# Kernel optimization log

Measured on AMD Instinct MI355X. Metric: run time of the kernel, lower is better.

The kernel has to match this reference:

```python
import jax, jax.numpy as jnp
import numpy as np

H = 256  # GRU hidden size (self.dim)

def setup_inputs() -> dict:
    key = jax.random.key(0)
    ks = jax.random.split(key, 7)
    B, T, N_IN, N_C = 256, 512, 512, 101
    s_ih = 1.0 / np.sqrt(H)
    x    = jax.random.normal(ks[0], (B, T, N_IN), dtype=jnp.float32)
    W_ih = jax.random.uniform(ks[1], (3 * H, N_IN), minval=-s_ih, maxval=s_ih, dtype=jnp.float32)
    W_hh = jax.random.uniform(ks[2], (3 * H, H),    minval=-s_ih, maxval=s_ih, dtype=jnp.float32)
    b_ih = jax.random.uniform(ks[3], (3 * H,), minval=-s_ih, maxval=s_ih, dtype=jnp.float32)
    b_hh = jax.random.uniform(ks[4], (3 * H,), minval=-s_ih, maxval=s_ih, dtype=jnp.float32)
    s_fc = 1.0 / np.sqrt(H)
    fc_w = jax.random.uniform(ks[5], (N_C, H), minval=-s_fc, maxval=s_fc, dtype=jnp.float32)
    fc_b = jax.random.uniform(ks[6], (N_C,),   minval=-s_fc, maxval=s_fc, dtype=jnp.float32)
    return {"x": x, "W_ih": W_ih, "W_hh": W_hh, "b_ih": b_ih, "b_hh": b_hh,
            "fc_w": fc_w, "fc_b": fc_b}

def _gru_last_hidden(x, W_ih, W_hh, b_ih, b_hh):
    B = x.shape[0]
    # Precompute input-side gate projections for all timesteps: [B, T, 3H]
    xg = jnp.einsum('bti,gi->btg', x, W_ih) + b_ih
    h0 = jnp.zeros((B, H), dtype=x.dtype)

    def step(h, xg_t):
        hg = h @ W_hh.T + b_hh                      # [B, 3H]
        xr, xz, xn = jnp.split(xg_t, 3, axis=-1)    # PyTorch gate order: r, z, n
        hr, hz, hn = jnp.split(hg, 3, axis=-1)
        r = jax.nn.sigmoid(xr + hr)
        z = jax.nn.sigmoid(xz + hz)
        n = jnp.tanh(xn + r * hn)
        h_new = (1.0 - z) * n + z * h
        return h_new, None

    hT, _ = jax.lax.scan(step, h0, jnp.swapaxes(xg, 0, 1))  # scan over T
    return hT  # [B, H]

def reference(x, W_ih, W_hh, b_ih, b_hh, fc_w, fc_b):
    hT = _gru_last_hidden(x, W_ih, W_hh, b_ih, b_hh)
    return hT @ fc_w.T + fc_b  # [B, n_c]
```

## Files before the change

### kernel.cpp

```cpp
#include <hip/hip_runtime.h>
#include <hip/hip_bf16.h>
#include <cstdint>
#include <cstddef>

typedef __attribute__((ext_vector_type(4))) float floatx4;
typedef __attribute__((ext_vector_type(8))) short shortx8;
typedef __attribute__((ext_vector_type(2))) __fp16 f16x2;

#define T_SEQ 512
#define NIN   512
#define BATCH 256
#define HID   256
#define G3    768
#define NC    101

static __device__ __forceinline__ unsigned short f2bf(float f){
  unsigned int u = __float_as_uint(f);
  u += 0x7FFFu + ((u >> 16) & 1u);
  return (unsigned short)(u >> 16);
}

static __device__ __forceinline__ float dot2acc(f16x2 w, f16x2 h, float acc){
#if __has_builtin(__builtin_amdgcn_fdot2)
  return __builtin_amdgcn_fdot2(w, h, acc, false);
#else
  return acc + (float)w[0]*(float)h[0] + (float)w[1]*(float)h[1];
#endif
}

#define BM 128
#define BN 128
#define BK 64
#define LDK 72

__global__ __launch_bounds__(256) void gemm_xg(
    const float* __restrict__ x, const float* __restrict__ Wih,
    const float* __restrict__ bih, float* __restrict__ xg,
    int t0, int tcLog2)
{
  __shared__ unsigned short As[BM*LDK];
  __shared__ unsigned short Bs[BN*LDK];
  const int tid  = threadIdx.x;
  const int bn   = blockIdx.x;
  const int bm   = blockIdx.y;
  const int w    = tid >> 6;
  const int l    = tid & 63;
  const int lm   = l & 15;
  const int quad = l >> 4;

  const int srow = tid >> 4;
  const int scol = (tid & 15) * 4;
  const int tcMask = (1 << tcLog2) - 1;

  floatx4 acc[2][8];
  #pragma unroll
  for (int mt = 0; mt < 2; ++mt)
    #pragma unroll
    for (int nt = 0; nt < 8; ++nt)
      acc[mt][nt] = (floatx4){0.f, 0.f, 0.f, 0.f};

  for (int kt = 0; kt < NIN / BK; ++kt){
    const int k0 = kt * BK;
    __syncthreads();
    #pragma unroll
    for (int p = 0; p < 8; ++p){
      const int r  = p * 16 + srow;
      const int gm = bm * BM + r;
      const int b  = gm >> tcLog2;
      const int tt = gm & tcMask;
      const float4 xa = *(const float4*)(x + (size_t)(b * T_SEQ + t0 + tt) * NIN + k0 + scol);
      union { unsigned short u[4]; uint2 v; } pa;
      pa.u[0] = f2bf(xa.x); pa.u[1] = f2bf(xa.y); pa.u[2] = f2bf(xa.z); pa.u[3] = f2bf(xa.w);
      *(uint2*)&As[r * LDK + scol] = pa.v;
      const int gn = bn * BN + r;
      const float4 wb = *(const float4*)(Wih + (size_t)gn * NIN + k0 + scol);
      union { unsigned short u[4]; uint2 v; } pb;
      pb.u[0] = f2bf(wb.x); pb.u[1] = f2bf(wb.y); pb.u[2] = f2bf(wb.z); pb.u[3] = f2bf(wb.w);
      *(uint2*)&Bs[r * LDK + scol] = pb.v;
    }
    __syncthreads();
    #pragma unroll
    for (int ks = 0; ks < 2; ++ks){
      const int kk = ks * 32 + quad * 8;
      shortx8 af[2], bfr[8];
      #pragma unroll
      for (int mt = 0; mt < 2; ++mt)
        af[mt] = *(const shortx8*)&As[(w * 32 + mt * 16 + lm) * LDK + kk];
      #pragma unroll
      for (int nt = 0; nt < 8; ++nt)
        bfr[nt] = *(const shortx8*)&Bs[(nt * 16 + lm) * LDK + kk];
      #pragma unroll
      for (int mt = 0; mt < 2; ++mt)
        #pragma unroll
        for (int nt = 0; nt < 8; ++nt)
          acc[mt][nt] = __builtin_amdgcn_mfma_f32_16x16x32_bf16(af[mt], bfr[nt], acc[mt][nt], 0, 0, 0);
    }
  }

  #pragma unroll
  for (int mt = 0; mt < 2; ++mt){
    #pragma unroll
    for (int nt = 0; nt < 8; ++nt){
      #pragma unroll
      for (int i = 0; i < 4; ++i){
        const int ml = w * 32 + mt * 16 + quad * 4 + i;
        const int nl = nt * 16 + lm;
        const int gm = bm * BM + ml;
        const int gn = bn * BN + nl;
        xg[(size_t)gm * G3 + gn] = acc[mt][nt][i] + bih[gn];
      }
    }
  }
}

#define HSTRIDE 280

__global__ __launch_bounds__(512, 2) void gru_steps(
    const float* __restrict__ xg, const float* __restrict__ Whh,
    const float* __restrict__ bhh, float* __restrict__ hstate, int Tc)
{
  __shared__ alignas(16) unsigned short hph[2][HSTRIDE];
  const int b    = blockIdx.x;
  const int tid  = threadIdx.x;
  const int j    = tid >> 1;
  const int half = tid & 1;
  const int jpos = j + (j >= 128 ? 8 : 0);

  f16x2 wrr[64], wrz[64], wrn[64];
  {
    const float4* r4 = (const float4*)(Whh + (size_t)j * HID + half * 128);
    const float4* z4 = (const float4*)(Whh + (size_t)(j + 256) * HID + half * 128);
    const float4* n4 = (const float4*)(Whh + (size_t)(j + 512) * HID + half * 128);
    #pragma unroll
    for (int k = 0; k < 32; ++k){
      float4 v = r4[k];
      wrr[2*k]   = __builtin_amdgcn_cvt_pkrtz(v.x, v.y);
      wrr[2*k+1] = __builtin_amdgcn_cvt_pkrtz(v.z, v.w);
    }
    #pragma unroll
    for (int k = 0; k < 32; ++k){
      float4 v = z4[k];
      wrz[2*k]   = __builtin_amdgcn_cvt_pkrtz(v.x, v.y);
      wrz[2*k+1] = __builtin_amdgcn_cvt_pkrtz(v.z, v.w);
    }
    #pragma unroll
    for (int k = 0; k < 32; ++k){
      float4 v = n4[k];
      wrn[2*k]   = __builtin_amdgcn_cvt_pkrtz(v.x, v.y);
      wrn[2*k+1] = __builtin_amdgcn_cvt_pkrtz(v.z, v.w);
    }
  }
  const float br = bhh[j];
  const float bz = bhh[j + 256];
  const float bn = bhh[j + 512];

  float hj = hstate[b * HID + j];
  if (half == 0){
    union { __fp16 f; unsigned short u; } cv;
    cv.f = (__fp16)hj;
    hph[0][jpos] = cv.u;
  }
  __syncthreads();

  const float* xgrow = xg + (size_t)b * Tc * G3 + j;
  float xr = xgrow[0], xz = xgrow[256], xn = xgrow[512];

  #pragma unroll 1
  for (int t = 0; t < Tc; ++t){
    const int tn = (t + 1 < Tc) ? (t + 1) : t;
    const float nxr = xgrow[(size_t)tn * G3];
    const float nxz = xgrow[(size_t)tn * G3 + 256];
    const float nxn = xgrow[(size_t)tn * G3 + 512];

    const uint4* hp4 = (const uint4*)(&hph[t & 1][0]) + half * 17;
    uint4 hv[16];
    #pragma unroll
    for (int i = 0; i < 16; ++i) hv[i] = hp4[i];

    float ar = 0.f, az = 0.f, an = 0.f;
    #pragma unroll
    for (int i = 0; i < 16; ++i){
      union { unsigned int u; f16x2 h; } c0, c1, c2, c3;
      c0.u = hv[i].x; c1.u = hv[i].y; c2.u = hv[i].z; c3.u = hv[i].w;
      const int p = 4 * i;
      ar = dot2acc(wrr[p    ], c0.h, ar);
      az = dot2acc(wrz[p    ], c0.h, az);
      an = dot2acc(wrn[p    ], c0.h, an);
      ar = dot2acc(wrr[p + 1], c1.h, ar);
      az = dot2acc(wrz[p + 1], c1.h, az);
      an = dot2acc(wrn[p + 1], c1.h, an);
      ar = dot2acc(wrr[p + 2], c2.h, ar);
      az = dot2acc(wrz[p + 2], c2.h, az);
      an = dot2acc(wrn[p + 2], c2.h, an);
      ar = dot2acc(wrr[p + 3], c3.h, ar);
      az = dot2acc(wrz[p + 3], c3.h, az);
      an = dot2acc(wrn[p + 3], c3.h, an);
    }
    const float hr = ar + __shfl_xor(ar, 1, 64) + br;
    const float hz = az + __shfl_xor(az, 1, 64) + bz;
    const float hn = an + __shfl_xor(an, 1, 64) + bn;

    const float r = 1.f / (1.f + __expf(-(xr + hr)));
    const float z = 1.f / (1.f + __expf(-(xz + hz)));
    const float a = xn + r * hn;
    const float ex = __expf(-2.f * fabsf(a));
    float n = (1.f - ex) / (1.f + ex);
    n = copysignf(n, a);
    const float hnew = fmaf(z, hj - n, n);

    hj = hnew;
    if (half == 0){
      union { __fp16 f; unsigned short u; } cv;
      cv.f = (__fp16)hj;
      hph[1 - (t & 1)][jpos] = cv.u;
    }
    __syncthreads();
    xr = nxr; xz = nxz; xn = nxn;
  }

  if (half == 0) hstate[b * HID + j] = hj;
}

__global__ __launch_bounds__(128) void fc_kernel(
    const float* __restrict__ hstate, const float* __restrict__ fw,
    const float* __restrict__ fb, float* __restrict__ out)
{
  __shared__ float hs[HID];
  const int b = blockIdx.x;
  const int t = threadIdx.x;
  hs[t]       = hstate[b * HID + t];
  hs[t + 128] = hstate[b * HID + t + 128];
  __syncthreads();
  if (t < NC){
    float acc = fb[t];
    const float4* w4 = (const float4*)(fw + (size_t)t * HID);
    const float4* h4 = (const float4*)hs;
    #pragma unroll
    for (int k = 0; k < 64; ++k){
      const float4 wv = w4[k];
      const float4 hv = h4[k];
      acc += wv.x * hv.x + wv.y * hv.y + wv.z * hv.z + wv.w * hv.w;
    }
    out[b * NC + t] = acc;
  }
}

extern "C" void kernel_launch(void* const* d_in, const int* in_sizes, int n_in,
                              void* d_out, int out_size, void* d_ws, size_t ws_size,
                              hipStream_t stream)
{
  const float* x   = (const float*)d_in[0];
  const float* Wih = (const float*)d_in[1];
  const float* Whh = (const float*)d_in[2];
  const float* bih = (const float*)d_in[3];
  const float* bhh = (const float*)d_in[4];
  const float* fcw = (const float*)d_in[5];
  const float* fcb = (const float*)d_in[6];
  float* out = (float*)d_out;

  float* hst = (float*)d_ws;
  const size_t hBytes = (size_t)BATCH * HID * sizeof(float);
  float* xg  = (float*)((char*)d_ws + hBytes);

  const size_t perT = (size_t)BATCH * G3 * sizeof(float);
  const size_t avail = (ws_size > hBytes) ? (ws_size - hBytes) : 0;
  int tcLog2 = 9;
  while (tcLog2 > 0 && perT * ((size_t)1 << tcLog2) > avail) --tcLog2;
  const int Tc = 1 << tcLog2;

  (void)hipMemsetAsync(hst, 0, hBytes, stream);
  for (int t0 = 0; t0 < T_SEQ; t0 += Tc){
    dim3 grid(6, 2 * Tc);
    gemm_xg<<<grid, 256, 0, stream>>>(x, Wih, bih, xg, t0, tcLog2);
    gru_steps<<<BATCH, 512, 0, stream>>>(xg, Whh, bhh, hst, Tc);
  }
  fc_kernel<<<BATCH, 128, 0, stream>>>(hst, fcw, fcb, out);
}
```

Before: 1.281 ms.

## Split GRU recurrent dot products across four lanes with DPP reduction

Reworks the per-step recurrent matvec so each group of four lanes computes two hidden units. Each lane covers a 64-wide K slice and the partial sums are combined with two DPP adds instead of one ds_swizzle shuffle. Each lane now reads half as much of the f16 hidden state from LDS per step, and each h value is reused across six weight rows instead of three. The cost is more duplicated work: every lane computes six accumulators and redundant gate math for two outputs, and the LDS padding layout changes.

```diff
diff --git a/kernel.cpp b/kernel.cpp
--- a/kernel.cpp
+++ b/kernel.cpp
@@ -26,6 +26,12 @@
 #else
   return acc + (float)w[0]*(float)h[0] + (float)w[1]*(float)h[1];
 #endif
+}
+
+template<int CTRL>
+static __device__ __forceinline__ float dppadd(float v){
+  return v + __int_as_float(__builtin_amdgcn_update_dpp(
+      0, __float_as_int(v), CTRL, 0xF, 0xF, true));
 }
 
 #define BM 128
@@ -120,85 +126,110 @@
     const float* __restrict__ bhh, float* __restrict__ hstate, int Tc)
 {
   __shared__ alignas(16) unsigned short hph[2][HSTRIDE];
-  const int b    = blockIdx.x;
-  const int tid  = threadIdx.x;
-  const int j    = tid >> 1;
-  const int half = tid & 1;
-  const int jpos = j + (j >= 128 ? 8 : 0);
-
-  f16x2 wrr[64], wrz[64], wrn[64];
+  const int b   = blockIdx.x;
+  const int tid = threadIdx.x;
+  const int q   = tid & 3;
+  const int g   = tid >> 2;
+  const int sel = q >> 1;
+  const int jm  = g + (sel << 7);
+  const int k0  = q << 6;
+
+  f16x2 w0r[32], w0z[32], w0n[32], w1r[32], w1z[32], w1n[32];
   {
-    const float4* r4 = (const float4*)(Whh + (size_t)j * HID + half * 128);
-    const float4* z4 = (const float4*)(Whh + (size_t)(j + 256) * HID + half * 128);
-    const float4* n4 = (const float4*)(Whh + (size_t)(j + 512) * HID + half * 128);
-    #pragma unroll
-    for (int k = 0; k < 32; ++k){
-      float4 v = r4[k];
-      wrr[2*k]   = __builtin_amdgcn_cvt_pkrtz(v.x, v.y);
-      wrr[2*k+1] = __builtin_amdgcn_cvt_pkrtz(v.z, v.w);
-    }
-    #pragma unroll
-    for (int k = 0; k < 32; ++k){
-      float4 v = z4[k];
-      wrz[2*k]   = __builtin_amdgcn_cvt_pkrtz(v.x, v.y);
-      wrz[2*k+1] = __builtin_amdgcn_cvt_pkrtz(v.z, v.w);
-    }
-    #pragma unroll
-    for (int k = 0; k < 32; ++k){
-      float4 v = n4[k];
-      wrn[2*k]   = __builtin_amdgcn_cvt_pkrtz(v.x, v.y);
-      wrn[2*k+1] = __builtin_amdgcn_cvt_pkrtz(v.z, v.w);
-    }
-  }
-  const float br = bhh[j];
-  const float bz = bhh[j + 256];
-  const float bn = bhh[j + 512];
-
-  float hj = hstate[b * HID + j];
-  if (half == 0){
+    const float4* p0 = (const float4*)(Whh + (size_t)(g      ) * HID + k0);
+    #pragma unroll
+    for (int k = 0; k < 16; ++k){ float4 v = p0[k];
+      w0r[2*k] = __builtin_amdgcn_cvt_pkrtz(v.x, v.y); w0r[2*k+1] = __builtin_amdgcn_cvt_pkrtz(v.z, v.w); }
+    const float4* p1 = (const float4*)(Whh + (size_t)(g + 256) * HID + k0);
+    #pragma unroll
+    for (int k = 0; k < 16; ++k){ float4 v = p1[k];
+      w0z[2*k] = __builtin_amdgcn_cvt_pkrtz(v.x, v.y); w0z[2*k+1] = __builtin_amdgcn_cvt_pkrtz(v.z, v.w); }
+    const float4* p2 = (const float4*)(Whh + (size_t)(g + 512) * HID + k0);
+    #pragma unroll
+    for (int k = 0; k < 16; ++k){ float4 v = p2[k];
+      w0n[2*k] = __builtin_amdgcn_cvt_pkrtz(v.x, v.y); w0n[2*k+1] = __builtin_amdgcn_cvt_pkrtz(v.z, v.w); }
+    const float4* p3 = (const float4*)(Whh + (size_t)(g + 128) * HID + k0);
+    #pragma unroll
+    for (int k = 0; k < 16; ++k){ float4 v = p3[k];
+      w1r[2*k] = __builtin_amdgcn_cvt_pkrtz(v.x, v.y); w1r[2*k+1] = __builtin_amdgcn_cvt_pkrtz(v.z, v.w); }
+    const float4* p4 = (const float4*)(Whh + (size_t)(g + 384) * HID + k0);
+    #pragma unroll
+    for (int k = 0; k < 16; ++k){ float4 v = p4[k];
+      w1z[2*k] = __builtin_amdgcn_cvt_pkrtz(v.x, v.y); w1z[2*k+1] = __builtin_amdgcn_cvt_pkrtz(v.z, v.w); }
+    const float4* p5 = (const float4*)(Whh + (size_t)(g + 640) * HID + k0);
+    #pragma unroll
+    for (int k = 0; k < 16; ++k){ float4 v = p5[k];
+      w1n[2*k] = __builtin_amdgcn_cvt_pkrtz(v.x, v.y); w1n[2*k+1] = __builtin_amdgcn_cvt_pkrtz(v.z, v.w); }
+  }
+  const float br = bhh[jm];
+  const float bz = bhh[jm + 256];
+  const float bn = bhh[jm + 512];
+
+  float hj = hstate[b * HID + jm];
+  const int wpos = jm + ((jm >> 6) << 3);
+  if (!(q & 1)){
     union { __fp16 f; unsigned short u; } cv;
     cv.f = (__fp16)hj;
-    hph[0][jpos] = cv.u;
+    hph[0][wpos] = cv.u;
   }
   __syncthreads();
 
-  const float* xgrow = xg + (size_t)b * Tc * G3 + j;
-  float xr = xgrow[0], xz = xgrow[256], xn = xgrow[512];
+  const int xbase = b * Tc * G3 + jm;
+  float xr = xg[xbase], xz = xg[xbase + 256], xn = xg[xbase + 512];
 
   #pragma unroll 1
   for (int t = 0; t < Tc; ++t){
     const int tn = (t + 1 < Tc) ? (t + 1) : t;
-    const float nxr = xgrow[(size_t)tn * G3];
-    const float nxz = xgrow[(size_t)tn * G3 + 256];
-    const float nxn = xgrow[(size_t)tn * G3 + 512];
-
-    const uint4* hp4 = (const uint4*)(&hph[t & 1][0]) + half * 17;
-    uint4 hv[16];
-    #pragma unroll
-    for (int i = 0; i < 16; ++i) hv[i] = hp4[i];
-
-    float ar = 0.f, az = 0.f, an = 0.f;
-    #pragma unroll
-    for (int i = 0; i < 16; ++i){
+    const int xo = xbase + tn * G3;
+    const float nxr = xg[xo];
+    const float nxz = xg[xo + 256];
+    const float nxn = xg[xo + 512];
+
+    const uint4* hp4 = (const uint4*)(&hph[t & 1][0]) + 9 * q;
+    uint4 hv[8];
+    #pragma unroll
+    for (int i = 0; i < 8; ++i) hv[i] = hp4[i];
+
+    float a0r = 0.f, a0z = 0.f, a0n = 0.f, a1r = 0.f, a1z = 0.f, a1n = 0.f;
+    #pragma unroll
+    for (int i = 0; i < 8; ++i){
       union { unsigned int u; f16x2 h; } c0, c1, c2, c3;
       c0.u = hv[i].x; c1.u = hv[i].y; c2.u = hv[i].z; c3.u = hv[i].w;
       const int p = 4 * i;
-      ar = dot2acc(wrr[p    ], c0.h, ar);
-      az = dot2acc(wrz[p    ], c0.h, az);
-      an = dot2acc(wrn[p    ], c0.h, an);
-      ar = dot2acc(wrr[p + 1], c1.h, ar);
-      az = dot2acc(wrz[p + 1], c1.h, az);
-      an = dot2acc(wrn[p + 1], c1.h, an);
-      ar = dot2acc(wrr[p + 2], c2.h, ar);
-      az = dot2acc(wrz[p + 2], c2.h, az);
-      an = dot2acc(wrn[p + 2], c2.h, an);
-      ar = dot2acc(wrr[p + 3], c3.h, ar);
-      az = dot2acc(wrz[p + 3], c3.h, az);
-      an = dot2acc(wrn[p + 3], c3.h, an);
-    }
-    const float hr = ar + __shfl_xor(ar, 1, 64) + br;
-    const float hz = az + __shfl_xor(az, 1, 64) + bz;
-    const float hn = an + __shfl_xor(an, 1, 64) + bn;
+      a0r = dot2acc(w0r[p    ], c0.h, a0r);
+      a0z = dot2acc(w0z[p    ], c0.h, a0z);
+      a0n = dot2acc(w0n[p    ], c0.h, a0n);
+      a1r = dot2acc(w1r[p    ], c0.h, a1r);
+      a1z = dot2acc(w1z[p    ], c0.h, a1z);
+      a1n = dot2acc(w1n[p    ], c0.h, a1n);
+      a0r = dot2acc(w0r[p + 1], c1.h, a0r);
+      a0z = dot2acc(w0z[p + 1], c1.h, a0z);
+      a0n = dot2acc(w0n[p + 1], c1.h, a0n);
+      a1r = dot2acc(w1r[p + 1], c1.h, a1r);
+      a1z = dot2acc(w1z[p + 1], c1.h, a1z);
+      a1n = dot2acc(w1n[p + 1], c1.h, a1n);
+      a0r = dot2acc(w0r[p + 2], c2.h, a0r);
+      a0z = dot2acc(w0z[p + 2], c2.h, a0z);
+      a0n = dot2acc(w0n[p + 2], c2.h, a0n);
+      a1r = dot2acc(w1r[p + 2], c2.h, a1r);
+      a1z = dot2acc(w1z[p + 2], c2.h, a1z);
+      a1n = dot2acc(w1n[p + 2], c2.h, a1n);
+      a0r = dot2acc(w0r[p + 3], c3.h, a0r);
+      a0z = dot2acc(w0z[p + 3], c3.h, a0z);
+      a0n = dot2acc(w0n[p + 3], c3.h, a0n);
+      a1r = dot2acc(w1r[p + 3], c3.h, a1r);
+      a1z = dot2acc(w1z[p + 3], c3.h, a1z);
+      a1n = dot2acc(w1n[p + 3], c3.h, a1n);
+    }
+
+    a0r = dppadd<0xB1>(a0r); a0z = dppadd<0xB1>(a0z); a0n = dppadd<0xB1>(a0n);
+    a1r = dppadd<0xB1>(a1r); a1z = dppadd<0xB1>(a1z); a1n = dppadd<0xB1>(a1n);
+    a0r = dppadd<0x4E>(a0r); a0z = dppadd<0x4E>(a0z); a0n = dppadd<0x4E>(a0n);
+    a1r = dppadd<0x4E>(a1r); a1z = dppadd<0x4E>(a1z); a1n = dppadd<0x4E>(a1n);
+
+    const float hr = (sel ? a1r : a0r) + br;
+    const float hz = (sel ? a1z : a0z) + bz;
+    const float hn = (sel ? a1n : a0n) + bn;
 
     const float r = 1.f / (1.f + __expf(-(xr + hr)));
     const float z = 1.f / (1.f + __expf(-(xz + hz)));
@@ -209,16 +240,16 @@
     const float hnew = fmaf(z, hj - n, n);
 
     hj = hnew;
-    if (half == 0){
+    if (!(q & 1)){
       union { __fp16 f; unsigned short u; } cv;
       cv.f = (__fp16)hj;
-      hph[1 - (t & 1)][jpos] = cv.u;
+      hph[1 - (t & 1)][wpos] = cv.u;
     }
     __syncthreads();
     xr = nxr; xz = nxz; xn = nxn;
   }
 
-  if (half == 0) hstate[b * HID + j] = hj;
+  if (!(q & 1)) hstate[b * HID + jm] = hj;
 }
 
 __global__ __launch_bounds__(128) void fc_kernel(
```

Result: faster. 1.255 ms (-2.0%).

## Batch GRU recurrence over 16 sequences per block using MFMA, store xg in fp16

Applied to the files above, without the earlier changes.

Replaces the per-sequence dot2 recurrence (one block per batch row) with a block that handles 16 batch rows and computes the hidden-to-hidden product with 16x16x32 f16 MFMA. W_hh fragments stay in registers and h is kept swizzled in LDS. The input projection buffer is also written in fp16, halving its memory traffic. Only 16 blocks now run the recurrence, so parallelism drops sharply and per-step latency becomes the deciding cost. fp16 storage of xg also adds rounding error.

```diff
diff --git a/kernel.cpp b/kernel.cpp
--- a/kernel.cpp
+++ b/kernel.cpp
@@ -1,11 +1,13 @@
 #include <hip/hip_runtime.h>
 #include <hip/hip_bf16.h>
+#include <hip/hip_fp16.h>
 #include <cstdint>
 #include <cstddef>
 
 typedef __attribute__((ext_vector_type(4))) float floatx4;
 typedef __attribute__((ext_vector_type(8))) short shortx8;
 typedef __attribute__((ext_vector_type(2))) __fp16 f16x2;
+typedef __attribute__((ext_vector_type(8))) __fp16 halfx8;
 
 #define T_SEQ 512
 #define NIN   512
@@ -20,14 +22,6 @@
   return (unsigned short)(u >> 16);
 }
 
-static __device__ __forceinline__ float dot2acc(f16x2 w, f16x2 h, float acc){
-#if __has_builtin(__builtin_amdgcn_fdot2)
-  return __builtin_amdgcn_fdot2(w, h, acc, false);
-#else
-  return acc + (float)w[0]*(float)h[0] + (float)w[1]*(float)h[1];
-#endif
-}
-
 #define BM 128
 #define BN 128
 #define BK 64
@@ -35,7 +29,7 @@
 
 __global__ __launch_bounds__(256) void gemm_xg(
     const float* __restrict__ x, const float* __restrict__ Wih,
-    const float* __restrict__ bih, float* __restrict__ xg,
+    const float* __restrict__ bih, __fp16* __restrict__ xg,
     int t0, int tcLog2)
 {
   __shared__ unsigned short As[BM*LDK];
@@ -107,118 +101,135 @@
         const int nl = nt * 16 + lm;
         const int gm = bm * BM + ml;
         const int gn = bn * BN + nl;
-        xg[(size_t)gm * G3 + gn] = acc[mt][nt][i] + bih[gn];
+        xg[(size_t)gm * G3 + gn] = (__fp16)(acc[mt][nt][i] + bih[gn]);
       }
     }
   }
 }
 
-#define HSTRIDE 280
-
-__global__ __launch_bounds__(512, 2) void gru_steps(
-    const float* __restrict__ xg, const float* __restrict__ Whh,
+#define BB 16
+
+__global__ __launch_bounds__(512, 2) void gru_mfma(
+    const __fp16* __restrict__ xg, const float* __restrict__ Whh,
     const float* __restrict__ bhh, float* __restrict__ hstate, int Tc)
 {
-  __shared__ alignas(16) unsigned short hph[2][HSTRIDE];
-  const int b    = blockIdx.x;
-  const int tid  = threadIdx.x;
-  const int j    = tid >> 1;
-  const int half = tid & 1;
-  const int jpos = j + (j >= 128 ? 8 : 0);
-
-  f16x2 wrr[64], wrz[64], wrn[64];
-  {
-    const float4* r4 = (const float4*)(Whh + (size_t)j * HID + half * 128);
-    const float4* z4 = (const float4*)(Whh + (size_t)(j + 256) * HID + half * 128);
-    const float4* n4 = (const float4*)(Whh + (size_t)(j + 512) * HID + half * 128);
-    #pragma unroll
-    for (int k = 0; k < 32; ++k){
-      float4 v = r4[k];
-      wrr[2*k]   = __builtin_amdgcn_cvt_pkrtz(v.x, v.y);
-      wrr[2*k+1] = __builtin_amdgcn_cvt_pkrtz(v.z, v.w);
-    }
-    #pragma unroll
-    for (int k = 0; k < 32; ++k){
-      float4 v = z4[k];
-      wrz[2*k]   = __builtin_amdgcn_cvt_pkrtz(v.x, v.y);
-      wrz[2*k+1] = __builtin_amdgcn_cvt_pkrtz(v.z, v.w);
-    }
-    #pragma unroll
-    for (int k = 0; k < 32; ++k){
-      float4 v = n4[k];
-      wrn[2*k]   = __builtin_amdgcn_cvt_pkrtz(v.x, v.y);
-      wrn[2*k+1] = __builtin_amdgcn_cvt_pkrtz(v.z, v.w);
-    }
-  }
-  const float br = bhh[j];
-  const float bz = bhh[j + 256];
-  const float bn = bhh[j + 512];
-
-  float hj = hstate[b * HID + j];
-  if (half == 0){
-    union { __fp16 f; unsigned short u; } cv;
-    cv.f = (__fp16)hj;
-    hph[0][jpos] = cv.u;
-  }
+  __shared__ __align__(16) __fp16 hls[2][BB * HID];
+  const int tid = threadIdx.x;
+  const int w   = tid >> 6;
+  const int l   = tid & 63;
+  const int lm  = l & 15;
+  const int lq  = l >> 4;
+  const int bb0 = blockIdx.x * BB;
+  const int jb  = w * 32 + lm;
+  const int hswz = (lm & 7) << 3;
+
+  halfx8 Bf[3][2][8];
+  #pragma unroll
+  for (int g = 0; g < 3; ++g)
+    #pragma unroll
+    for (int js = 0; js < 2; ++js)
+      #pragma unroll
+      for (int ks = 0; ks < 8; ++ks){
+        const float* wp = Whh + (size_t)(g * 256 + w * 32 + js * 16 + lm) * HID + ks * 32 + lq * 8;
+        const float4 v0 = *(const float4*)wp;
+        const float4 v1 = *(const float4*)(wp + 4);
+        union { f16x2 h[4]; halfx8 v; } u;
+        u.h[0] = __builtin_amdgcn_cvt_pkrtz(v0.x, v0.y);
+        u.h[1] = __builtin_amdgcn_cvt_pkrtz(v0.z, v0.w);
+        u.h[2] = __builtin_amdgcn_cvt_pkrtz(v1.x, v1.y);
+        u.h[3] = __builtin_amdgcn_cvt_pkrtz(v1.z, v1.w);
+        Bf[g][js][ks] = u.v;
+      }
+
+  float bias[3][2];
+  #pragma unroll
+  for (int g = 0; g < 3; ++g){
+    bias[g][0] = bhh[g * 256 + jb];
+    bias[g][1] = bhh[g * 256 + jb + 16];
+  }
+
+  float hold[2][4];
+  #pragma unroll
+  for (int js = 0; js < 2; ++js)
+    #pragma unroll
+    for (int i = 0; i < 4; ++i){
+      const int b = lq * 4 + i;
+      const int j = jb + js * 16;
+      const float h0 = hstate[(bb0 + b) * HID + j];
+      hold[js][i] = h0;
+      hls[0][b * HID + (j ^ ((b & 7) << 3))] = (__fp16)h0;
+    }
+
+  int rowoff[4];
+  #pragma unroll
+  for (int i = 0; i < 4; ++i)
+    rowoff[i] = ((bb0 + lq * 4 + i) * Tc) * G3 + jb;
+
   __syncthreads();
-
-  const float* xgrow = xg + (size_t)b * Tc * G3 + j;
-  float xr = xgrow[0], xz = xgrow[256], xn = xgrow[512];
 
   #pragma unroll 1
   for (int t = 0; t < Tc; ++t){
-    const int tn = (t + 1 < Tc) ? (t + 1) : t;
-    const float nxr = xgrow[(size_t)tn * G3];
-    const float nxz = xgrow[(size_t)tn * G3 + 256];
-    const float nxn = xgrow[(size_t)tn * G3 + 512];
-
-    const uint4* hp4 = (const uint4*)(&hph[t & 1][0]) + half * 17;
-    uint4 hv[16];
-    #pragma unroll
-    for (int i = 0; i < 16; ++i) hv[i] = hp4[i];
-
-    float ar = 0.f, az = 0.f, an = 0.f;
-    #pragma unroll
-    for (int i = 0; i < 16; ++i){
-      union { unsigned int u; f16x2 h; } c0, c1, c2, c3;
-      c0.u = hv[i].x; c1.u = hv[i].y; c2.u = hv[i].z; c3.u = hv[i].w;
-      const int p = 4 * i;
-      ar = dot2acc(wrr[p    ], c0.h, ar);
-      az = dot2acc(wrz[p    ], c0.h, az);
-      an = dot2acc(wrn[p    ], c0.h, an);
-      ar = dot2acc(wrr[p + 1], c1.h, ar);
-      az = dot2acc(wrz[p + 1], c1.h, az);
-      an = dot2acc(wrn[p + 1], c1.h, an);
-      ar = dot2acc(wrr[p + 2], c2.h, ar);
-      az = dot2acc(wrz[p + 2], c2.h, az);
-      an = dot2acc(wrn[p + 2], c2.h, an);
-      ar = dot2acc(wrr[p + 3], c3.h, ar);
-      az = dot2acc(wrz[p + 3], c3.h, az);
-      an = dot2acc(wrn[p + 3], c3.h, an);
-    }
-    const float hr = ar + __shfl_xor(ar, 1, 64) + br;
-    const float hz = az + __shfl_xor(az, 1, 64) + bz;
-    const float hn = an + __shfl_xor(an, 1, 64) + bn;
-
-    const float r = 1.f / (1.f + __expf(-(xr + hr)));
-    const float z = 1.f / (1.f + __expf(-(xz + hz)));
-    const float a = xn + r * hn;
-    const float ex = __expf(-2.f * fabsf(a));
-    float n = (1.f - ex) / (1.f + ex);
-    n = copysignf(n, a);
-    const float hnew = fmaf(z, hj - n, n);
-
-    hj = hnew;
-    if (half == 0){
-      union { __fp16 f; unsigned short u; } cv;
-      cv.f = (__fp16)hj;
-      hph[1 - (t & 1)][jpos] = cv.u;
-    }
+    __fp16 xv[3][2][4];
+    #pragma unroll
+    for (int i = 0; i < 4; ++i){
+      const __fp16* xp = xg + rowoff[i] + t * G3;
+      #pragma unroll
+      for (int g = 0; g < 3; ++g)
+        #pragma unroll
+        for (int js = 0; js < 2; ++js)
+          xv[g][js][i] = xp[g * 256 + js * 16];
+    }
+
+    floatx4 acc[3][2];
+    #pragma unroll
+    for (int g = 0; g < 3; ++g)
+      #pragma unroll
+      for (int js = 0; js < 2; ++js)
+        acc[g][js] = (floatx4){bias[g][js], bias[g][js], bias[g][js], bias[g][js]};
+
+    const __fp16* hb = &hls[t & 1][0];
+    #pragma unroll
+    for (int ks = 0; ks < 8; ++ks){
+      const int off = (ks * 32 + lq * 8) ^ hswz;
+      const halfx8 av = *(const halfx8*)&hb[lm * HID + off];
+      #pragma unroll
+      for (int g = 0; g < 3; ++g)
+        #pragma unroll
+        for (int js = 0; js < 2; ++js)
+          acc[g][js] = __builtin_amdgcn_mfma_f32_16x16x32_f16(av, Bf[g][js][ks], acc[g][js], 0, 0, 0);
+    }
+
+    __fp16* hbn = &hls[(t + 1) & 1][0];
+    #pragma unroll
+    for (int js = 0; js < 2; ++js)
+      #pragma unroll
+      for (int i = 0; i < 4; ++i){
+        const float ar = acc[0][js][i];
+        const float az = acc[1][js][i];
+        const float an = acc[2][js][i];
+        const float xr = (float)xv[0][js][i];
+        const float xz = (float)xv[1][js][i];
+        const float xn = (float)xv[2][js][i];
+        const float r = 1.f / (1.f + __expf(-(xr + ar)));
+        const float z = 1.f / (1.f + __expf(-(xz + az)));
+        const float a = xn + r * an;
+        const float ex = __expf(-2.f * fabsf(a));
+        float n = (1.f - ex) / (1.f + ex);
+        n = copysignf(n, a);
+        const float hnew = fmaf(z, hold[js][i] - n, n);
+        hold[js][i] = hnew;
+        const int b = lq * 4 + i;
+        const int j = jb + js * 16;
+        hbn[b * HID + (j ^ ((b & 7) << 3))] = (__fp16)hnew;
+      }
     __syncthreads();
-    xr = nxr; xz = nxz; xn = nxn;
-  }
-
-  if (half == 0) hstate[b * HID + j] = hj;
+  }
+
+  #pragma unroll
+  for (int js = 0; js < 2; ++js)
+    #pragma unroll
+    for (int i = 0; i < 4; ++i)
+      hstate[(bb0 + lq * 4 + i) * HID + jb + js * 16] = hold[js][i];
 }
 
 __global__ __launch_bounds__(128) void fc_kernel(
@@ -260,9 +271,9 @@
 
   float* hst = (float*)d_ws;
   const size_t hBytes = (size_t)BATCH * HID * sizeof(float);
-  float* xg  = (float*)((char*)d_ws + hBytes);
-
-  const size_t perT = (size_t)BATCH * G3 * sizeof(float);
+  __fp16* xg = (__fp16*)((char*)d_ws + hBytes);
+
+  const size_t perT = (size_t)BATCH * G3 * sizeof(__fp16);
   const size_t avail = (ws_size > hBytes) ? (ws_size - hBytes) : 0;
   int tcLog2 = 9;
   while (tcLog2 > 0 && perT * ((size_t)1 << tcLog2) > avail) --tcLog2;
@@ -272,7 +283,7 @@
   for (int t0 = 0; t0 < T_SEQ; t0 += Tc){
     dim3 grid(6, 2 * Tc);
     gemm_xg<<<grid, 256, 0, stream>>>(x, Wih, bih, xg, t0, tcLog2);
-    gru_steps<<<BATCH, 512, 0, stream>>>(xg, Whh, bhh, hst, Tc);
+    gru_mfma<<<BATCH / BB, 512, 0, stream>>>(xg, Whh, bhh, hst, Tc);
   }
   fc_kernel<<<BATCH, 128, 0, stream>>>(hst, fcw, fcb, out);
 }
```

Measured after the change: 4.069 ms. 3.18x slower.
